# Optimization experiments

Hardware: AMD Instinct MI355X
Metric: run time of the kernel (lower is better)

Reference implementation:

```python
import jax, jax.numpy as jnp
import numpy as np


def setup_inputs() -> dict:
    key = jax.random.key(0)
    k1, k2 = jax.random.split(key)
    B, IN, OUT = 4096, 4096, 4096
    x = jax.random.normal(k1, (B, IN), dtype=jnp.float32)
    W = jax.random.normal(k2, (OUT, IN), dtype=jnp.float32) * (1.0 / np.sqrt(IN))
    return {"x": x, "W": W, "k": 128}


def reference(x, W, k):
    # temp = (x[:, None, :] * W).sum(axis=1)  ==  x * W.sum(axis=0)  -> [B, in]
    # (the original materializes the O(B*out*in) intermediate; math is identical)
    temp = jax.lax.stop_gradient(x) * jnp.sum(W, axis=0)  # x_vals is detached in torch
    _, idx_top = jax.lax.top_k(jnp.abs(temp), k)          # [B, k] indices into `in` dim
    B = x.shape[0]
    z = jnp.ones_like(x).at[jnp.arange(B)[:, None], idx_top].set(0.0)
    out = jnp.matmul(x * z, W.T)                          # [B, out]
    return out
```

## Files before the change

kernel.cpp:

```cpp
#include <hip/hip_runtime.h>
#include <hip/hip_bf16.h>
#include <stdint.h>

#define B_DIM   4096
#define IN_DIM  4096
#define OUT_DIM 4096
#define K_SEL   128

typedef unsigned short u16;
typedef __bf16 bf16x8 __attribute__((ext_vector_type(8)));
typedef float  f32x4  __attribute__((ext_vector_type(4)));

static __device__ __forceinline__ u16 f2bf(float f) {
    uint32_t u = __builtin_bit_cast(uint32_t, f);
    uint32_t r = (u + 0x7fffu + ((u >> 16) & 1u)) >> 16;
    return (u16)r;
}

__global__ __launch_bounds__(256) void colsum_conv(const float* __restrict__ W,
                                                   double* __restrict__ part,
                                                   u16* __restrict__ Wb) {
    int cb = blockIdx.x & 3;
    int rb = blockIdx.x >> 2;
    int c4 = cb * 256 + threadIdx.x;
    int row0 = rb * 32;
    double s0 = 0.0, s1 = 0.0, s2 = 0.0, s3 = 0.0;
    for (int r = 0; r < 32; ++r) {
        const float4 v = ((const float4*)(W + (size_t)(row0 + r) * IN_DIM))[c4];
        s0 += (double)v.x; s1 += (double)v.y; s2 += (double)v.z; s3 += (double)v.w;
        ushort4 o;
        o.x = f2bf(v.x); o.y = f2bf(v.y); o.z = f2bf(v.z); o.w = f2bf(v.w);
        ((ushort4*)(Wb + (size_t)(row0 + r) * IN_DIM))[c4] = o;
    }
    double4 d; d.x = s0; d.y = s1; d.z = s2; d.w = s3;
    ((double4*)(part + (size_t)rb * IN_DIM))[c4] = d;
}

__global__ __launch_bounds__(256) void colsum_final(const double* __restrict__ part,
                                                    float* __restrict__ cs) {
    __shared__ double red[256];
    const int t = threadIdx.x;
    const int c = blockIdx.x * 16 + (t & 15);
    const int g = t >> 4;
    double s = 0.0;
    for (int r = 0; r < 8; ++r) s += part[(size_t)(g * 8 + r) * IN_DIM + c];
    red[t] = s;
    __syncthreads();
    for (int off = 128; off >= 16; off >>= 1) {
        if (t < off) red[t] += red[t + off];
        __syncthreads();
    }
    if (t < 16) cs[blockIdx.x * 16 + t] = (float)red[t];
}

__global__ __launch_bounds__(256) void topk_mask(const float* __restrict__ x,
                                                 const float* __restrict__ cs,
                                                 u16* __restrict__ xz) {
    __shared__ uint32_t hist[256];
    __shared__ uint32_t wtot[4];
    __shared__ uint32_t s_prefix, s_krem;

    const int b = blockIdx.x, t = threadIdx.x;
    const int lane = t & 63, wv = t >> 6;
    const float4* xrow = (const float4*)(x + (size_t)b * IN_DIM);
    const float4* csv  = (const float4*)cs;

    float    xr[16];
    uint32_t ul[16];
#pragma unroll
    for (int q = 0; q < 4; ++q) {
        float4 xv = xrow[t * 4 + q];
        float4 cv = csv[t * 4 + q];
        xr[q*4+0] = xv.x; xr[q*4+1] = xv.y; xr[q*4+2] = xv.z; xr[q*4+3] = xv.w;
        ul[q*4+0] = __builtin_bit_cast(uint32_t, xv.x * cv.x) & 0x7fffffffu;
        ul[q*4+1] = __builtin_bit_cast(uint32_t, xv.y * cv.y) & 0x7fffffffu;
        ul[q*4+2] = __builtin_bit_cast(uint32_t, xv.z * cv.z) & 0x7fffffffu;
        ul[q*4+3] = __builtin_bit_cast(uint32_t, xv.w * cv.w) & 0x7fffffffu;
    }
    if (t == 0) { s_prefix = 0u; s_krem = K_SEL; }
    __syncthreads();

#pragma unroll
    for (int p = 3; p >= 0; --p) {
        const int sh = p * 8;
        const uint32_t hi_mask = (p == 3) ? 0u : (0xFFFFFFFFu << (sh + 8));
        const uint32_t prefix = s_prefix;
        const uint32_t krem   = s_krem;
        hist[t] = 0u;
        __syncthreads();
#pragma unroll
        for (int j = 0; j < 16; ++j) {
            uint32_t u = ul[j];
            if ((u & hi_mask) == (prefix & hi_mask))
                atomicAdd(&hist[(u >> sh) & 255u], 1u);
        }
        __syncthreads();
        const uint32_t h = hist[t];
        uint32_t v = h;
#pragma unroll
        for (int off = 1; off < 64; off <<= 1) {
            uint32_t got = __shfl_down(v, off);
            if (lane + off < 64) v += got;
        }
        if (lane == 0) wtot[wv] = v;
        __syncthreads();
        uint32_t add = 0;
#pragma unroll
        for (int ww = 0; ww < 4; ++ww)
            if (ww > wv) add += wtot[ww];
        const uint32_t mysuf   = v + add;
        const uint32_t nextsuf = mysuf - h;
        if (mysuf >= krem && nextsuf < krem) {
            s_prefix = prefix | ((uint32_t)t << sh);
            s_krem   = krem - nextsuf;
        }
        __syncthreads();
    }
    const uint32_t T       = s_prefix;
    const uint32_t need_eq = s_krem;

    uint32_t cnt = 0;
#pragma unroll
    for (int j = 0; j < 16; ++j) cnt += (ul[j] == T) ? 1u : 0u;
    uint32_t inc = cnt;
#pragma unroll
    for (int off = 1; off < 64; off <<= 1) {
        uint32_t got = __shfl_up(inc, off);
        if (lane >= off) inc += got;
    }
    if (lane == 63) wtot[wv] = inc;
    __syncthreads();
    uint32_t wbase = 0;
#pragma unroll
    for (int ww = 0; ww < 4; ++ww)
        if (ww < wv) wbase += wtot[ww];
    const int base = (int)(inc + wbase - cnt);

    union { u16 us[16]; uint4 v4[2]; } ob;
    int eqseen = 0;
#pragma unroll
    for (int j = 0; j < 16; ++j) {
        uint32_t u = ul[j];
        bool drop = (u > T);
        if (u == T) {
            if (base + eqseen < (int)need_eq) drop = true;
            ++eqseen;
        }
        ob.us[j] = drop ? (u16)0 : f2bf(xr[j]);
    }
    uint4* dst = (uint4*)(xz + (size_t)b * IN_DIM + t * 16);
    dst[0] = ob.v4[0];
    dst[1] = ob.v4[1];
}

#define NT 64

__global__ __launch_bounds__(512, 2) void gemm_pl(const u16* __restrict__ A,
                                                  const u16* __restrict__ Bm,
                                                  float* __restrict__ C) {
    __shared__ u16 lds_[65536];

    const int bid = blockIdx.x;
    const int swz = (bid & 7) * 32 + (bid >> 3);
    const int m0 = (swz >> 4) * 256, n0 = (swz & 15) * 256;

    const int t = threadIdx.x;
    const int l = t & 63;
    const int lr = l & 15, lk = l >> 4;
    const int w = t >> 6;
    const int wm = w >> 2, wn = w & 3;

    const int cswz = ((t & 7) ^ ((t >> 3) & 7)) * 8;
    const int c0   = (lk ^ (lr & 7)) * 8;
    const int c1   = c0 ^ 32;

    f32x4 acc[8][4];
#pragma unroll
    for (int i = 0; i < 8; ++i)
#pragma unroll
        for (int j = 0; j < 4; ++j) acc[i][j] = f32x4{0.f, 0.f, 0.f, 0.f};

#define GLOAD(g, off_bytes)                                                     \
    __builtin_amdgcn_global_load_lds(                                           \
        (const __attribute__((address_space(1))) void*)(g),                     \
        (__attribute__((address_space(3))) void*)(((char*)lds_) + (off_bytes)), \
        16, 0, 0)

    auto stA = [&](int kb, int r, int kt) {
#pragma unroll
        for (int g = 0; g < 2; ++g)
            GLOAD(A + (size_t)(m0 + g * 128 + r * 64 + (t >> 3)) * IN_DIM + kt + cswz,
                  kb * 65536 + r * 16384 + g * 8192 + t * 16);
    };
    auto stB = [&](int kb, int r, int kt) {
#pragma unroll
        for (int g = 0; g < 2; ++g)
            GLOAD(Bm + (size_t)(n0 + r * 128 + g * 64 + (t >> 3)) * IN_DIM + kt + cswz,
                  kb * 65536 + 32768 + r * 16384 + g * 8192 + t * 16);
    };

    auto rdA = [&](bf16x8 (&dst)[4], int bufo, int qm, int c) {
#pragma unroll
        for (int mi = 0; mi < 4; ++mi)
            dst[mi] = *(const bf16x8*)&lds_[bufo + qm * 8192 + wm * 4096 + lr * 64 + mi * 1024 + c];
    };
    auto rdB = [&](bf16x8 (&dst)[4], int bufo, int c) {
#pragma unroll
        for (int ni = 0; ni < 4; ++ni)
            dst[ni] = *(const bf16x8*)&lds_[bufo + 16384 + (wn >> 1) * 8192 + (wn & 1) * 4096 + lr * 64 + ni * 1024 + c];
    };
    auto mm = [&](int base, bf16x8 (&Aa)[4], bf16x8 (&Bb)[4]) {
        __builtin_amdgcn_s_setprio(1);
#pragma unroll
        for (int mi = 0; mi < 4; ++mi)
#pragma unroll
            for (int ni = 0; ni < 4; ++ni)
                acc[base + mi][ni] = __builtin_amdgcn_mfma_f32_16x16x32_bf16(
                    Aa[mi], Bb[ni], acc[base + mi][ni], 0, 0, 0);
        __builtin_amdgcn_s_setprio(0);
        __builtin_amdgcn_sched_barrier(0);
    };

    bf16x8 a0k0[4], a0k1[4], a1k0[4], a1k1[4], bk0[4], bk1[4];

    stA(0, 0, 0); stA(0, 1, 0); stB(0, 0, 0); stB(0, 1, 0);
    stA(1, 0, 64); stB(1, 0, 64); stB(1, 1, 64);
    asm volatile("s_waitcnt vmcnt(6)" ::: "memory");
    __builtin_amdgcn_s_barrier();
    asm volatile("" ::: "memory");
    rdA(a0k0, 0, 0, c0);
    rdB(bk0, 0, c0);

    for (int k = 0; k < NT; ++k) {
        const int bufo = (k & 1) * 32768;
        const int bufno = bufo ^ 32768;
        const int kbC = k & 1, kbN = kbC ^ 1;
        const int kt1 = (k + 1) * 64, kt2 = (k + 2) * 64;

        rdA(a0k1, bufo, 0, c1);
        rdB(bk1, bufo, c1);
        if (k < NT - 1) stA(kbN, 1, kt1);
        mm(0, a0k0, bk0);

        rdA(a1k0, bufo, 1, c0);
        rdA(a1k1, bufo, 1, c1);
        mm(0, a0k1, bk1);
        asm volatile("" ::: "memory");
        __builtin_amdgcn_s_barrier();
        asm volatile("" ::: "memory");

        if (k < NT - 2) { stA(kbC, 0, kt2); stB(kbC, 0, kt2); }
        mm(4, a1k0, bk0);
        if (k < NT - 2) {
            asm volatile("s_waitcnt vmcnt(4)" ::: "memory");
        } else {
            asm volatile("s_waitcnt vmcnt(0)" ::: "memory");
        }
        __builtin_amdgcn_s_barrier();
        asm volatile("" ::: "memory");

        if (k < NT - 1) {
            rdA(a0k0, bufno, 0, c0);
            rdB(bk0, bufno, c0);
        }
        if (k < NT - 2) stB(kbC, 1, kt2);
        mm(4, a1k1, bk1);
    }
#undef GLOAD

#pragma unroll
    for (int gmi = 0; gmi < 8; ++gmi)
#pragma unroll
        for (int ni = 0; ni < 4; ++ni)
#pragma unroll
            for (int r = 0; r < 4; ++r) {
                int row = m0 + wm * 128 + (gmi >> 2) * 64 + (gmi & 3) * 16 + lk * 4 + r;
                int col = n0 + wn * 64 + ni * 16 + lr;
                C[(size_t)row * OUT_DIM + col] = acc[gmi][ni][r];
            }
}

extern "C" void kernel_launch(void* const* d_in, const int* in_sizes, int n_in,
                              void* d_out, int out_size, void* d_ws, size_t ws_size,
                              hipStream_t stream) {
    const float* x = (const float*)d_in[0];
    const float* W = (const float*)d_in[1];
    float* out = (float*)d_out;

    char* ws = (char*)d_ws;
    u16*    Wb   = (u16*)ws;
    u16*    xz   = (u16*)(ws + (size_t)32 * 1024 * 1024);
    float*  cs   = (float*)(ws + (size_t)64 * 1024 * 1024);
    double* part = (double*)d_out;

    colsum_conv<<<512, 256, 0, stream>>>(W, part, Wb);
    colsum_final<<<256, 256, 0, stream>>>(part, cs);
    topk_mask<<<4096, 256, 0, stream>>>(x, cs, xz);
    gemm_pl<<<256, 512, 0, stream>>>(xz, Wb, out);
}
```

Baseline: 178.2 us.

## Switch GEMM to 32x32x16 MFMA tiles and split column-sum over more blocks

The GEMM inner loop moves from 16x16x32 bf16 MFMA to 32x32x16 bf16 MFMA. This changes the per-wave register tiling, the LDS read pattern with its swizzled k-columns, and the epilogue row/column mapping. The larger MFMA shape needs fewer LDS fragment reads per flop and issues fewer instructions. Separately, colsum_conv is launched with four times as many blocks, each covering 8 rows, and colsum_final now reduces 512 partial rows instead of 128, trading more partial-sum traffic for more parallelism in the W conversion pass.

```diff
diff --git a/kernel.cpp b/kernel.cpp
--- a/kernel.cpp
+++ b/kernel.cpp
@@ -9,7 +9,7 @@
 
 typedef unsigned short u16;
 typedef __bf16 bf16x8 __attribute__((ext_vector_type(8)));
-typedef float  f32x4  __attribute__((ext_vector_type(4)));
+typedef float  f32x16 __attribute__((ext_vector_type(16)));
 
 static __device__ __forceinline__ u16 f2bf(float f) {
     uint32_t u = __builtin_bit_cast(uint32_t, f);
@@ -23,9 +23,9 @@
     int cb = blockIdx.x & 3;
     int rb = blockIdx.x >> 2;
     int c4 = cb * 256 + threadIdx.x;
-    int row0 = rb * 32;
+    int row0 = rb * 8;
     double s0 = 0.0, s1 = 0.0, s2 = 0.0, s3 = 0.0;
-    for (int r = 0; r < 32; ++r) {
+    for (int r = 0; r < 8; ++r) {
         const float4 v = ((const float4*)(W + (size_t)(row0 + r) * IN_DIM))[c4];
         s0 += (double)v.x; s1 += (double)v.y; s2 += (double)v.z; s3 += (double)v.w;
         ushort4 o;
@@ -43,7 +43,7 @@
     const int c = blockIdx.x * 16 + (t & 15);
     const int g = t >> 4;
     double s = 0.0;
-    for (int r = 0; r < 8; ++r) s += part[(size_t)(g * 8 + r) * IN_DIM + c];
+    for (int r = 0; r < 32; ++r) s += part[(size_t)(g * 32 + r) * IN_DIM + c];
     red[t] = s;
     __syncthreads();
     for (int off = 128; off >= 16; off >>= 1) {
@@ -166,19 +166,24 @@
 
     const int t = threadIdx.x;
     const int l = t & 63;
-    const int lr = l & 15, lk = l >> 4;
     const int w = t >> 6;
     const int wm = w >> 2, wn = w & 3;
+    const int r31 = l & 31;
+    const int jb  = l >> 5;
+    const int x7  = l & 7;
 
     const int cswz = ((t & 7) ^ ((t >> 3) & 7)) * 8;
-    const int c0   = (lk ^ (lr & 7)) * 8;
-    const int c1   = c0 ^ 32;
-
-    f32x4 acc[8][4];
-#pragma unroll
-    for (int i = 0; i < 8; ++i)
-#pragma unroll
-        for (int j = 0; j < 4; ++j) acc[i][j] = f32x4{0.f, 0.f, 0.f, 0.f};
+    int kcol[4];
+#pragma unroll
+    for (int ks = 0; ks < 4; ++ks) kcol[ks] = ((ks * 2 + jb) ^ x7) * 8;
+
+    f32x16 acc[4][2];
+#pragma unroll
+    for (int i = 0; i < 4; ++i)
+#pragma unroll
+        for (int j = 0; j < 2; ++j)
+#pragma unroll
+            for (int e = 0; e < 16; ++e) acc[i][j][e] = 0.f;
 
 #define GLOAD(g, off_bytes)                                                     \
     __builtin_amdgcn_global_load_lds(                                           \
@@ -199,37 +204,45 @@
                   kb * 65536 + 32768 + r * 16384 + g * 8192 + t * 16);
     };
 
-    auto rdA = [&](bf16x8 (&dst)[4], int bufo, int qm, int c) {
-#pragma unroll
-        for (int mi = 0; mi < 4; ++mi)
-            dst[mi] = *(const bf16x8*)&lds_[bufo + qm * 8192 + wm * 4096 + lr * 64 + mi * 1024 + c];
-    };
-    auto rdB = [&](bf16x8 (&dst)[4], int bufo, int c) {
-#pragma unroll
-        for (int ni = 0; ni < 4; ++ni)
-            dst[ni] = *(const bf16x8*)&lds_[bufo + 16384 + (wn >> 1) * 8192 + (wn & 1) * 4096 + lr * 64 + ni * 1024 + c];
-    };
-    auto mm = [&](int base, bf16x8 (&Aa)[4], bf16x8 (&Bb)[4]) {
+    auto rdA = [&](bf16x8 (&dst)[2][2], int bufo, int qm, int kh) {
+#pragma unroll
+        for (int m2 = 0; m2 < 2; ++m2)
+#pragma unroll
+            for (int ki = 0; ki < 2; ++ki)
+                dst[m2][ki] = *(const bf16x8*)&lds_[bufo + qm * 8192 + wm * 4096
+                    + (m2 * 32 + r31) * 64 + kcol[kh * 2 + ki]];
+    };
+    auto rdB = [&](bf16x8 (&dst)[2][2], int bufo, int kh) {
+#pragma unroll
+        for (int n2 = 0; n2 < 2; ++n2)
+#pragma unroll
+            for (int ki = 0; ki < 2; ++ki)
+                dst[n2][ki] = *(const bf16x8*)&lds_[bufo + 16384 + (wn >> 1) * 8192
+                    + (wn & 1) * 4096 + (n2 * 32 + r31) * 64 + kcol[kh * 2 + ki]];
+    };
+    auto mm = [&](int qm, bf16x8 (&Aa)[2][2], bf16x8 (&Bb)[2][2]) {
         __builtin_amdgcn_s_setprio(1);
 #pragma unroll
-        for (int mi = 0; mi < 4; ++mi)
-#pragma unroll
-            for (int ni = 0; ni < 4; ++ni)
-                acc[base + mi][ni] = __builtin_amdgcn_mfma_f32_16x16x32_bf16(
-                    Aa[mi], Bb[ni], acc[base + mi][ni], 0, 0, 0);
+        for (int m2 = 0; m2 < 2; ++m2)
+#pragma unroll
+            for (int n2 = 0; n2 < 2; ++n2)
+#pragma unroll
+                for (int ki = 0; ki < 2; ++ki)
+                    acc[qm * 2 + m2][n2] = __builtin_amdgcn_mfma_f32_32x32x16_bf16(
+                        Aa[m2][ki], Bb[n2][ki], acc[qm * 2 + m2][n2], 0, 0, 0);
         __builtin_amdgcn_s_setprio(0);
         __builtin_amdgcn_sched_barrier(0);
     };
 
-    bf16x8 a0k0[4], a0k1[4], a1k0[4], a1k1[4], bk0[4], bk1[4];
+    bf16x8 a0k0[2][2], a0k1[2][2], a1k0[2][2], a1k1[2][2], bk0[2][2], bk1[2][2];
 
     stA(0, 0, 0); stA(0, 1, 0); stB(0, 0, 0); stB(0, 1, 0);
     stA(1, 0, 64); stB(1, 0, 64); stB(1, 1, 64);
     asm volatile("s_waitcnt vmcnt(6)" ::: "memory");
     __builtin_amdgcn_s_barrier();
     asm volatile("" ::: "memory");
-    rdA(a0k0, 0, 0, c0);
-    rdB(bk0, 0, c0);
+    rdA(a0k0, 0, 0, 0);
+    rdB(bk0, 0, 0);
 
     for (int k = 0; k < NT; ++k) {
         const int bufo = (k & 1) * 32768;
@@ -237,20 +250,20 @@
         const int kbC = k & 1, kbN = kbC ^ 1;
         const int kt1 = (k + 1) * 64, kt2 = (k + 2) * 64;
 
-        rdA(a0k1, bufo, 0, c1);
-        rdB(bk1, bufo, c1);
+        rdA(a0k1, bufo, 0, 1);
+        rdB(bk1, bufo, 1);
         if (k < NT - 1) stA(kbN, 1, kt1);
         mm(0, a0k0, bk0);
 
-        rdA(a1k0, bufo, 1, c0);
-        rdA(a1k1, bufo, 1, c1);
+        rdA(a1k0, bufo, 1, 0);
+        rdA(a1k1, bufo, 1, 1);
         mm(0, a0k1, bk1);
         asm volatile("" ::: "memory");
         __builtin_amdgcn_s_barrier();
         asm volatile("" ::: "memory");
 
         if (k < NT - 2) { stA(kbC, 0, kt2); stB(kbC, 0, kt2); }
-        mm(4, a1k0, bk0);
+        mm(1, a1k0, bk0);
         if (k < NT - 2) {
             asm volatile("s_waitcnt vmcnt(4)" ::: "memory");
         } else {
@@ -260,23 +273,23 @@
         asm volatile("" ::: "memory");
 
         if (k < NT - 1) {
-            rdA(a0k0, bufno, 0, c0);
-            rdB(bk0, bufno, c0);
+            rdA(a0k0, bufno, 0, 0);
+            rdB(bk0, bufno, 0);
         }
         if (k < NT - 2) stB(kbC, 1, kt2);
-        mm(4, a1k1, bk1);
+        mm(1, a1k1, bk1);
     }
 #undef GLOAD
 
 #pragma unroll
-    for (int gmi = 0; gmi < 8; ++gmi)
-#pragma unroll
-        for (int ni = 0; ni < 4; ++ni)
-#pragma unroll
-            for (int r = 0; r < 4; ++r) {
-                int row = m0 + wm * 128 + (gmi >> 2) * 64 + (gmi & 3) * 16 + lk * 4 + r;
-                int col = n0 + wn * 64 + ni * 16 + lr;
-                C[(size_t)row * OUT_DIM + col] = acc[gmi][ni][r];
+    for (int mt = 0; mt < 4; ++mt)
+#pragma unroll
+        for (int nt = 0; nt < 2; ++nt)
+#pragma unroll
+            for (int r = 0; r < 16; ++r) {
+                int row = m0 + wm * 128 + mt * 32 + (r & 3) + 8 * (r >> 2) + 4 * (l >> 5);
+                int col = n0 + wn * 64 + nt * 32 + r31;
+                C[(size_t)row * OUT_DIM + col] = acc[mt][nt][r];
             }
 }
 
@@ -293,7 +306,7 @@
     float*  cs   = (float*)(ws + (size_t)64 * 1024 * 1024);
     double* part = (double*)d_out;
 
-    colsum_conv<<<512, 256, 0, stream>>>(W, part, Wb);
+    colsum_conv<<<2048, 256, 0, stream>>>(W, part, Wb);
     colsum_final<<<256, 256, 0, stream>>>(part, cs);
     topk_mask<<<4096, 256, 0, stream>>>(x, cs, xz);
     gemm_pl<<<256, 512, 0, stream>>>(xz, Wb, out);
```

Result: slower. 195.2 us (+9.5%).
